# Optimization experiments

Hardware: AMD Instinct MI355X
Metric: run time of the kernel (lower is better)

The kernel has to match this reference:

```python
import jax, jax.numpy as jnp
import numpy as np
import math

N_HEADS = 32
N_KV_HEADS = 8
HEAD_DIM = 64
THETA = 10000.0
NEG_INF = -1e9


def _rope_cos_sin(seq_len, dim, dtype=jnp.float32):
    # freqs over even indices, matching torch.arange(0, dim, 2)/dim
    freqs = 1.0 / (THETA ** (jnp.arange(0, dim, 2, dtype=jnp.float32) / dim))  # [dim/2]
    angles = jnp.arange(seq_len, dtype=jnp.float32)[:, None] * freqs[None, :]  # [S, dim/2]
    return jnp.cos(angles).astype(dtype), jnp.sin(angles).astype(dtype)


def _apply_rope(x, cos, sin):
    # x: [B, S, H, D]; pairs (x[...,2i], x[...,2i+1]) rotated as complex numbers
    xr = x[..., 0::2]
    xi = x[..., 1::2]
    # broadcast cos/sin [S, D/2] -> [1, S, 1, D/2]
    c = cos[None, :, None, :]
    s = sin[None, :, None, :]
    or_ = xr * c - xi * s
    oi_ = xr * s + xi * c
    # interleave back: [..., D/2, 2] -> [..., D]
    return jnp.stack([or_, oi_], axis=-1).reshape(x.shape)


def setup_inputs() -> dict:
    key = jax.random.key(0)
    ks = jax.random.split(key, 5)
    B, S, D = 2, 2048, 2048
    KV_D = N_KV_HEADS * HEAD_DIM
    x = jax.random.normal(ks[0], (B, S, D), dtype=jnp.float32)
    sc = 1.0 / math.sqrt(D)
    wq = jax.random.normal(ks[1], (D, D), dtype=jnp.float32) * sc
    wk = jax.random.normal(ks[2], (D, KV_D), dtype=jnp.float32) * sc
    wv = jax.random.normal(ks[3], (D, KV_D), dtype=jnp.float32) * sc
    wo = jax.random.normal(ks[4], (D, D), dtype=jnp.float32) * sc
    # additive causal mask [1, 1, S, S]
    causal = jnp.tril(jnp.ones((S, S), dtype=bool))
    mask = jnp.where(causal, 0.0, NEG_INF).astype(jnp.float32)[None, None]
    return {"x": x, "mask": mask, "wq": wq, "wk": wk, "wv": wv, "wo": wo}


def reference(x, mask, wq, wk, wv, wo):
    B, S, D = x.shape
    n_rep = N_HEADS // N_KV_HEADS
    q = (x @ wq).reshape(B, S, N_HEADS, HEAD_DIM)
    k = (x @ wk).reshape(B, S, N_KV_HEADS, HEAD_DIM)
    v = (x @ wv).reshape(B, S, N_KV_HEADS, HEAD_DIM)
    cos, sin = _rope_cos_sin(S, HEAD_DIM)
    q = _apply_rope(q, cos, sin)
    k = _apply_rope(k, cos, sin)
    # GQA: repeat_interleave kv heads along head dim
    k = jnp.repeat(k, n_rep, axis=2)  # [B, S, H, D]
    v = jnp.repeat(v, n_rep, axis=2)
    scores = jnp.einsum("bqhd,bkhd->bhqk", q, k) / math.sqrt(HEAD_DIM)
    scores = scores + mask
    probs = jax.nn.softmax(scores.astype(jnp.float32), axis=-1).astype(q.dtype)
    out = jnp.einsum("bhqk,bkhd->bqhd", probs, v).reshape(B, S, N_HEADS * HEAD_DIM)
    return out @ wo
```

## Files before the change

kernel.cpp:

```cpp
#include <hip/hip_runtime.h>
#include <hip/hip_bf16.h>


#define S_LEN 2048
#define BATCH 2
#define D_MODEL 2048
#define NH 32
#define NKV 8
#define HD 64
#define KV_D (NKV * HD)
#define QKV_N (D_MODEL + 2 * KV_D)

typedef __attribute__((ext_vector_type(8))) short short8;
typedef __attribute__((ext_vector_type(4))) float float4v;
typedef __attribute__((ext_vector_type(16))) float f32x16;
typedef __attribute__((ext_vector_type(2))) unsigned uint2v;

typedef __attribute__((address_space(1))) const unsigned int gu32;
typedef __attribute__((address_space(3))) unsigned int lu32;

#if __has_builtin(__builtin_amdgcn_exp2f)
#define PEXP(x) __builtin_amdgcn_exp2f(x)
#else
#define PEXP(x) __expf((x) * 0.69314718f)
#endif
#define QSCALE 0.18033688f

__device__ __forceinline__ float bf2f(unsigned short u) {
    unsigned x = ((unsigned)u) << 16;
    return __builtin_bit_cast(float, x);
}
__device__ __forceinline__ unsigned short f2bf(float f) {
    unsigned u = __builtin_bit_cast(unsigned, f);
    unsigned r = (u + 0x7fffu + ((u >> 16) & 1u)) >> 16;
    return (unsigned short)r;
}

__device__ __forceinline__ unsigned cvt_pk_bf16(float a, float b) {
    unsigned r;
    asm("v_cvt_pk_bf16_f32 %0, %1, %2" : "=v"(r) : "v"(a), "v"(b));
    return r;
}

__device__ __forceinline__ void pl32swap(unsigned a, unsigned b,
                                         unsigned& x, unsigned& y) {
#if __has_builtin(__builtin_amdgcn_permlane32_swap)
    uint2v r = __builtin_amdgcn_permlane32_swap(a, b, false, false);
    x = r[0];
    y = r[1];
#else
    unsigned pa = (unsigned)__shfl_xor((int)a, 32);
    unsigned pb = (unsigned)__shfl_xor((int)b, 32);
    bool lo = (threadIdx.x & 63) < 32;
    x = lo ? a : pb;
    y = lo ? pa : b;
#endif
}

__global__ __launch_bounds__(256) void prep(const float* __restrict__ x,
                                            const float* __restrict__ wq,
                                            const float* __restrict__ wk,
                                            const float* __restrict__ wv,
                                            const float* __restrict__ wo,
                                            unsigned short* __restrict__ xb,
                                            unsigned short* __restrict__ wqkvT,
                                            unsigned short* __restrict__ woT) {
    __shared__ unsigned short t[32 * 33];
    const int bx = blockIdx.x;
    if (bx >= 10240) {
        long i = ((long)(bx - 10240) * 256 + threadIdx.x) * 4;
        const long n = (long)BATCH * S_LEN * D_MODEL;
        if (i + 3 >= n) return;
        const float4v v = *(const float4v*)&x[i];
        unsigned short o[4];
        o[0] = f2bf(v[0]); o[1] = f2bf(v[1]); o[2] = f2bf(v[2]); o[3] = f2bf(v[3]);
        *(__attribute__((ext_vector_type(4))) short*)&xb[i] =
            *(__attribute__((ext_vector_type(4))) short*)o;
        return;
    }
    const float* in;
    unsigned short* out;
    int N, nb, kb;
    if (bx < 4096) {
        in = wq; out = wqkvT; N = 2048;
        nb = (bx & 63) * 32; kb = (bx >> 6) * 32;
    } else if (bx < 5120) {
        const int i2 = bx - 4096;
        in = wk; out = wqkvT + (long)D_MODEL * D_MODEL; N = 512;
        nb = (i2 & 15) * 32; kb = (i2 >> 4) * 32;
    } else if (bx < 6144) {
        const int i2 = bx - 5120;
        in = wv; out = wqkvT + (long)(D_MODEL + KV_D) * D_MODEL; N = 512;
        nb = (i2 & 15) * 32; kb = (i2 >> 4) * 32;
    } else {
        const int i2 = bx - 6144;
        in = wo; out = woT; N = 2048;
        nb = (i2 & 63) * 32; kb = (i2 >> 6) * 32;
    }
    const int c = threadIdx.x & 31, rr = threadIdx.x >> 5;
#pragma unroll
    for (int it = 0; it < 4; ++it) {
        int r = it * 8 + rr;
        t[c * 33 + r] = f2bf(in[(long)(kb + r) * N + nb + c]);
    }
    __syncthreads();
#pragma unroll
    for (int it = 0; it < 4; ++it) {
        int r = it * 8 + rr;
        out[(long)(nb + r) * D_MODEL + kb + c] = t[r * 33 + c];
    }
}

template <int TM, bool F32OUT>
__global__ __launch_bounds__(256, TM == 64 ? 4 : 3)
void gemm_sw(const unsigned short* __restrict__ A,
             const unsigned short* __restrict__ BT,
             void* __restrict__ Cv, int M, int N, int K) {
    __shared__ unsigned short As[TM * 64];
    __shared__ unsigned short Bs[128 * 64];
    const int tid = threadIdx.x;
    const int wid = tid >> 6, lane = tid & 63;
    const int l15 = lane & 15, quad = lane >> 4;
    const int wm = (wid >> 1) * (TM / 2), wn = (wid & 1) * 64;
    const int row0 = blockIdx.x * TM, col0 = blockIdx.y * 128;
    constexpr int MI = TM / 32;

    float4v acc[MI][4];
    float4v z;
    z[0] = z[1] = z[2] = z[3] = 0.0f;
    for (int mi = 0; mi < MI; ++mi)
        for (int ni = 0; ni < 4; ++ni) acc[mi][ni] = z;

    const int r_ld = lane >> 3;
    const int swz_ld = ((lane & 7) ^ (lane >> 3)) * 8;
    const int sw = l15 & 7;

    for (int kb = 0; kb < K; kb += 64) {
        __syncthreads();
#pragma unroll
        for (int c = 0; c < 4; ++c) {
            int chunk = c * 4 + wid;
            int r = chunk * 8 + r_ld;
            __builtin_amdgcn_global_load_lds(
                (gu32*)&BT[(long)(col0 + r) * K + kb + swz_ld],
                (lu32*)&Bs[chunk * 512], 16, 0, 0);
            if (c < MI)
                __builtin_amdgcn_global_load_lds(
                    (gu32*)&A[(long)(row0 + r) * K + kb + swz_ld],
                    (lu32*)&As[chunk * 512], 16, 0, 0);
        }
        __syncthreads();
#pragma unroll
        for (int kk = 0; kk < 64; kk += 32) {
            short8 af[MI], bf[4];
#pragma unroll
            for (int i = 0; i < MI; ++i)
                af[i] = *(const short8*)
                    &As[(wm + i * 16 + l15) * 64 + ((((kk >> 3) + quad) ^ sw) << 3)];
#pragma unroll
            for (int i = 0; i < 4; ++i)
                bf[i] = *(const short8*)
                    &Bs[(wn + i * 16 + l15) * 64 + ((((kk >> 3) + quad) ^ sw) << 3)];
#pragma unroll
            for (int mi = 0; mi < MI; ++mi)
#pragma unroll
                for (int ni = 0; ni < 4; ++ni)
                    acc[mi][ni] = __builtin_amdgcn_mfma_f32_16x16x32_bf16(
                        af[mi], bf[ni], acc[mi][ni], 0, 0, 0);
        }
    }
#pragma unroll
    for (int mi = 0; mi < MI; ++mi)
#pragma unroll
        for (int ni = 0; ni < 4; ++ni)
#pragma unroll
            for (int r = 0; r < 4; ++r) {
                int m = row0 + wm + mi * 16 + quad * 4 + r;
                int n = col0 + wn + ni * 16 + l15;
                if (F32OUT)
                    ((float*)Cv)[(long)m * N + n] = acc[mi][ni][r];
                else
                    ((unsigned short*)Cv)[(long)m * N + n] = f2bf(acc[mi][ni][r]);
            }
}

__global__ __launch_bounds__(256) void rope_vtrans(unsigned short* __restrict__ qkv,
                                                   unsigned short* __restrict__ Vt) {
    __shared__ unsigned t[64 * 33];
    const int bx = blockIdx.x, tid = threadIdx.x;
    if (bx < 512) {
        const int i = tid & 31;
        const int row = bx * 8 + (tid >> 5);
        const int s = row & (S_LEN - 1);
        float freq = __expf(-0.28782313f * (float)i);
        float ang = (float)s * freq;
        float c = cosf(ang), sn = sinf(ang);
        unsigned* p = (unsigned*)qkv + ((long)row * QKV_N + 2 * i) / 2;
#pragma unroll
        for (int head = 0; head < 40; ++head) {
            const float qs = (head < 32) ? QSCALE : 1.0f;
            unsigned v = p[head * 32];
            float xr = bf2f((unsigned short)(v & 0xffff));
            float xi = bf2f((unsigned short)(v >> 16));
            unsigned short lo = f2bf((xr * c - xi * sn) * qs);
            unsigned short hi = f2bf((xr * sn + xi * c) * qs);
            p[head * 32] = (unsigned)lo | ((unsigned)hi << 16);
        }
        return;
    }
    const int idx = bx - 512;
    const int st = (idx & 31) * 64, kh = (idx >> 5) & 7, b = idx >> 8;
    {
        const int r2 = tid >> 3, dbase = (tid & 7) * 8;
        const unsigned short* src =
            qkv + ((long)(b * S_LEN + st + 2 * r2)) * QKV_N + D_MODEL + KV_D + kh * HD + dbase;
        short8 lo = *(const short8*)src;
        short8 hi = *(const short8*)(src + QKV_N);
#pragma unroll
        for (int j = 0; j < 8; ++j)
            t[(dbase + j) * 33 + r2] =
                (unsigned)(unsigned short)lo[j] | ((unsigned)(unsigned short)hi[j] << 16);
    }
    __syncthreads();
    {
        const int d = tid >> 2, sb = (tid & 3) * 8;
        unsigned short o[16];
#pragma unroll
        for (int jj = 0; jj < 8; ++jj) {
            unsigned v = t[d * 33 + sb + jj];
            o[2 * jj] = (unsigned short)(v & 0xffff);
            o[2 * jj + 1] = (unsigned short)(v >> 16);
        }
        unsigned short* dst =
            Vt + ((long)((b * 8 + kh) * 64 + d)) * S_LEN + st + sb * 2;
        *(short8*)dst = *(short8*)&o[0];
        *(short8*)(dst + 8) = *(short8*)&o[8];
    }
}

__global__ __launch_bounds__(512, 4) void flash8(const unsigned short* __restrict__ qkv,
                                                 const unsigned short* __restrict__ Vt,
                                                 unsigned short* __restrict__ O) {
    __shared__ unsigned short Ks[4][64 * 64];
    __shared__ unsigned short Vs[4][64 * 64];

    const int tid = threadIdx.x, w = tid >> 6, lane = tid & 63;
    const int g = w & 3, p = w >> 2;
    const int l31 = lane & 31, hi = lane >> 5;
    const int r7 = l31 & 7;
    const int h = blockIdx.y, b = blockIdx.z;
    const int kh = h >> 2, bkh = b * 8 + kh;
    const int qtA = blockIdx.x;

    const int sr = lane >> 3;
    const int sc = ((lane & 7) ^ sr) * 8;
    const unsigned short* Kg =
        qkv + (long)b * S_LEN * QKV_N + D_MODEL + kh * HD + sc;
    const unsigned short* Vg = Vt + ((long)bkh * 64) * S_LEN + sc;

#define STAGE8(pb)                                                                   \
    do {                                                                             \
        const int tt = (pb) + p;                                                     \
        const int bt = tt & 3;                                                       \
        const long kk0 = (long)tt * 64;                                              \
        __builtin_amdgcn_global_load_lds(                                            \
            (gu32*)&Kg[(kk0 + g * 16 + sr) * QKV_N],                                 \
            (lu32*)&Ks[bt][(g * 16) * 64], 16, 0, 0);                                \
        __builtin_amdgcn_global_load_lds(                                            \
            (gu32*)&Kg[(kk0 + g * 16 + 8 + sr) * QKV_N],                             \
            (lu32*)&Ks[bt][(g * 16 + 8) * 64], 16, 0, 0);                            \
        __builtin_amdgcn_global_load_lds(                                            \
            (gu32*)&Vg[(long)(g * 16 + sr) * S_LEN + kk0],                           \
            (lu32*)&Vs[bt][(g * 16) * 64], 16, 0, 0);                                \
        __builtin_amdgcn_global_load_lds(                                            \
            (gu32*)&Vg[(long)(g * 16 + 8 + sr) * S_LEN + kk0],                       \
            (lu32*)&Vs[bt][(g * 16 + 8) * 64], 16, 0, 0);                            \
    } while (0)

    for (int tsel = 0; tsel < 2; ++tsel) {
        const int qt = tsel ? (15 - qtA) : qtA;
        const int row_w = qt * 128 + g * 32;
        const int nkt = 2 * qt + 2;
        const int nss = nkt >> 1;

        short8 aq[4];
        {
            const long qbase = ((long)(b * S_LEN) + row_w + l31) * QKV_N + h * HD + hi * 8;
#pragma unroll
            for (int ks = 0; ks < 4; ++ks) aq[ks] = *(const short8*)&qkv[qbase + ks * 16];
        }

        f32x16 oacc[2] = {};
        float lp = 0.0f;

        STAGE8(0);
        __syncthreads();

        for (int ss = 0; ss < nss; ++ss) {
            const int t = 2 * ss + p;
            const int k0 = t * 64;
            const int bt = t & 3;
            if (2 * ss + 2 < nkt) STAGE8(2 * ss + 2);

            if (row_w + 31 >= k0) {
                const bool mb = (k0 + 63 > row_w);
#pragma unroll
                for (int kb2 = 0; kb2 < 2; ++kb2) {
                    short8 kf[4];
#pragma unroll
                    for (int ks = 0; ks < 4; ++ks)
                        kf[ks] = *(const short8*)
                            &Ks[bt][(kb2 * 32 + l31) * 64 + (((ks * 2 + hi) ^ r7) << 3)];
                    f32x16 s = {};
                    __builtin_amdgcn_s_setprio(1);
#pragma unroll
                    for (int ks = 0; ks < 4; ++ks)
                        s = __builtin_amdgcn_mfma_f32_32x32x16_bf16(kf[ks], aq[ks], s, 0, 0, 0);
                    __builtin_amdgcn_s_setprio(0);

                    const int qrel = row_w + l31 - k0 - kb2 * 32 - 4 * hi;
#pragma unroll
                    for (int r = 0; r < 16; ++r) {
                        float v = s[r];
                        if (mb && ((r & 3) + 8 * (r >> 2) > qrel)) v = -1e4f;
                        float pv = PEXP(v);
                        lp += pv;
                        s[r] = pv;
                    }

#pragma unroll
                    for (int ksl = 0; ksl < 2; ++ksl) {
                        const int gx = ksl * 8;
                        unsigned ca = cvt_pk_bf16(s[gx + 0], s[gx + 1]);
                        unsigned cb = cvt_pk_bf16(s[gx + 2], s[gx + 3]);
                        unsigned cc = cvt_pk_bf16(s[gx + 4], s[gx + 5]);
                        unsigned cd = cvt_pk_bf16(s[gx + 6], s[gx + 7]);
                        unsigned dw0, dw1, dw2, dw3;
                        pl32swap(ca, cc, dw0, dw2);
                        pl32swap(cb, cd, dw1, dw3);
                        union { unsigned u[4]; short8 v8; } pf;
                        pf.u[0] = dw0; pf.u[1] = dw1; pf.u[2] = dw2; pf.u[3] = dw3;
                        const int lc = kb2 * 4 + ksl * 2 + hi;
                        __builtin_amdgcn_s_setprio(1);
#pragma unroll
                        for (int dblk = 0; dblk < 2; ++dblk) {
                            short8 vf = *(const short8*)
                                &Vs[bt][(dblk * 32 + l31) * 64 + ((lc ^ r7) << 3)];
                            oacc[dblk] = __builtin_amdgcn_mfma_f32_32x32x16_bf16(
                                vf, pf.v8, oacc[dblk], 0, 0, 0);
                        }
                        __builtin_amdgcn_s_setprio(0);
                    }
                }
            }
            __syncthreads();
        }

        float* mV = (float*)&Vs[0][0];
        float* mL = (float*)&Ks[2][0];
        if (p == 1) {
#pragma unroll
            for (int dblk = 0; dblk < 2; ++dblk)
#pragma unroll
                for (int r = 0; r < 16; ++r)
                    mV[(g * 32 + dblk * 16 + r) * 64 + lane] = oacc[dblk][r];
            mL[g * 64 + lane] = lp;
        }
        __syncthreads();
        if (p == 0) {
#pragma unroll
            for (int dblk = 0; dblk < 2; ++dblk)
#pragma unroll
                for (int r = 0; r < 16; ++r)
                    oacc[dblk][r] += mV[(g * 32 + dblk * 16 + r) * 64 + lane];
            lp += mL[g * 64 + lane];

            float linv = 1.0f / (lp + __shfl_xor(lp, 32));
            unsigned short* Oe = &Ks[0][0] + g * 2048;
#pragma unroll
            for (int dblk = 0; dblk < 2; ++dblk)
#pragma unroll
                for (int rq = 0; rq < 4; ++rq) {
                    unsigned plo = cvt_pk_bf16(oacc[dblk][rq * 4 + 0] * linv,
                                               oacc[dblk][rq * 4 + 1] * linv);
                    unsigned phi = cvt_pk_bf16(oacc[dblk][rq * 4 + 2] * linv,
                                               oacc[dblk][rq * 4 + 3] * linv);
                    uint2v wv;
                    wv[0] = plo; wv[1] = phi;
                    int e = l31 * 64 + (((rq + 4 * dblk) ^ r7) << 3) + hi * 4;
                    *(uint2v*)&Oe[e] = wv;
                }
#pragma unroll
            for (int i = 0; i < 4; ++i) {
                int q2 = i * 8 + (lane >> 3);
                int e = q2 * 64 + (((lane & 7) ^ (lane >> 3)) << 3);
                short8 ov = *(const short8*)&Oe[e];
                long orow = ((long)(b * S_LEN) + row_w + q2) * D_MODEL + h * HD + (lane & 7) * 8;
                *(short8*)&O[orow] = ov;
            }
        }
        __syncthreads();
    }
#undef STAGE8
}

extern "C" void kernel_launch(void* const* d_in, const int* in_sizes, int n_in,
                              void* d_out, int out_size, void* d_ws, size_t ws_size,
                              hipStream_t stream) {
    const float* x  = (const float*)d_in[0];
    const float* wq = (const float*)d_in[n_in - 4];
    const float* wk = (const float*)d_in[n_in - 3];
    const float* wv = (const float*)d_in[n_in - 2];
    const float* wo = (const float*)d_in[n_in - 1];
    float* out = (float*)d_out;

    unsigned short* ws    = (unsigned short*)d_ws;
    unsigned short* xb    = ws;
    unsigned short* Obuf  = ws;
    unsigned short* qkv   = xb + (long)BATCH * S_LEN * D_MODEL;
    unsigned short* woT   = qkv + (long)BATCH * S_LEN * QKV_N;
    unsigned short* wqkvT = woT + (long)D_MODEL * D_MODEL;
    unsigned short* Vt    = wqkvT;

    const int M = BATCH * S_LEN;

    prep<<<18432, 256, 0, stream>>>(x, wq, wk, wv, wo, xb, wqkvT, woT);

    gemm_sw<128, false><<<dim3(M / 128, QKV_N / 128), 256, 0, stream>>>(
        xb, wqkvT, qkv, M, QKV_N, D_MODEL);

    rope_vtrans<<<1024, 256, 0, stream>>>(qkv, Vt);

    flash8<<<dim3(8, NH, BATCH), 512, 0, stream>>>(qkv, Vt, Obuf);

    gemm_sw<128, true><<<dim3(M / 128, D_MODEL / 128), 256, 0, stream>>>(
        Obuf, woT, out, M, D_MODEL, D_MODEL);
}
```

Baseline: 289.2 us.

## Split flash attention KV tiles across four wave groups with tree reduction

```diff
diff --git a/kernel.cpp b/kernel.cpp
--- a/kernel.cpp
+++ b/kernel.cpp
@@ -238,11 +238,11 @@
     }
 }
 
-__global__ __launch_bounds__(512, 4) void flash8(const unsigned short* __restrict__ qkv,
-                                                 const unsigned short* __restrict__ Vt,
-                                                 unsigned short* __restrict__ O) {
-    __shared__ unsigned short Ks[4][64 * 64];
-    __shared__ unsigned short Vs[4][64 * 64];
+__global__ __launch_bounds__(1024, 8) void flash10(const unsigned short* __restrict__ qkv,
+                                                   const unsigned short* __restrict__ Vt,
+                                                   unsigned short* __restrict__ O) {
+    __shared__ unsigned short SM[8 * 4096];
+    __shared__ float mLs[768];
 
     const int tid = threadIdx.x, w = tid >> 6, lane = tid & 63;
     const int g = w & 3, p = w >> 2;
@@ -257,31 +257,14 @@
     const unsigned short* Kg =
         qkv + (long)b * S_LEN * QKV_N + D_MODEL + kh * HD + sc;
     const unsigned short* Vg = Vt + ((long)bkh * 64) * S_LEN + sc;
-
-#define STAGE8(pb)                                                                   \
-    do {                                                                             \
-        const int tt = (pb) + p;                                                     \
-        const int bt = tt & 3;                                                       \
-        const long kk0 = (long)tt * 64;                                              \
-        __builtin_amdgcn_global_load_lds(                                            \
-            (gu32*)&Kg[(kk0 + g * 16 + sr) * QKV_N],                                 \
-            (lu32*)&Ks[bt][(g * 16) * 64], 16, 0, 0);                                \
-        __builtin_amdgcn_global_load_lds(                                            \
-            (gu32*)&Kg[(kk0 + g * 16 + 8 + sr) * QKV_N],                             \
-            (lu32*)&Ks[bt][(g * 16 + 8) * 64], 16, 0, 0);                            \
-        __builtin_amdgcn_global_load_lds(                                            \
-            (gu32*)&Vg[(long)(g * 16 + sr) * S_LEN + kk0],                           \
-            (lu32*)&Vs[bt][(g * 16) * 64], 16, 0, 0);                                \
-        __builtin_amdgcn_global_load_lds(                                            \
-            (gu32*)&Vg[(long)(g * 16 + 8 + sr) * S_LEN + kk0],                       \
-            (lu32*)&Vs[bt][(g * 16 + 8) * 64], 16, 0, 0);                            \
-    } while (0)
+    unsigned short* const KB = &SM[p * 4096];
+    unsigned short* const VB = &SM[16384 + p * 4096];
 
     for (int tsel = 0; tsel < 2; ++tsel) {
         const int qt = tsel ? (15 - qtA) : qtA;
         const int row_w = qt * 128 + g * 32;
         const int nkt = 2 * qt + 2;
-        const int nss = nkt >> 1;
+        const int nss = (nkt + 3) >> 2;
 
         short8 aq[4];
         {
@@ -293,16 +276,27 @@
         f32x16 oacc[2] = {};
         float lp = 0.0f;
 
-        STAGE8(0);
-        __syncthreads();
-
         for (int ss = 0; ss < nss; ++ss) {
-            const int t = 2 * ss + p;
+            const int t = 4 * ss + p;
             const int k0 = t * 64;
-            const int bt = t & 3;
-            if (2 * ss + 2 < nkt) STAGE8(2 * ss + 2);
-
-            if (row_w + 31 >= k0) {
+            if (t < nkt) {
+                const long kk0 = (long)t * 64;
+                __builtin_amdgcn_global_load_lds(
+                    (gu32*)&Kg[(kk0 + g * 16 + sr) * QKV_N],
+                    (lu32*)&KB[(g * 16) * 64], 16, 0, 0);
+                __builtin_amdgcn_global_load_lds(
+                    (gu32*)&Kg[(kk0 + g * 16 + 8 + sr) * QKV_N],
+                    (lu32*)&KB[(g * 16 + 8) * 64], 16, 0, 0);
+                __builtin_amdgcn_global_load_lds(
+                    (gu32*)&Vg[(long)(g * 16 + sr) * S_LEN + kk0],
+                    (lu32*)&VB[(g * 16) * 64], 16, 0, 0);
+                __builtin_amdgcn_global_load_lds(
+                    (gu32*)&Vg[(long)(g * 16 + 8 + sr) * S_LEN + kk0],
+                    (lu32*)&VB[(g * 16 + 8) * 64], 16, 0, 0);
+            }
+            __syncthreads();
+
+            if (t < nkt && row_w + 31 >= k0) {
                 const bool mb = (k0 + 63 > row_w);
 #pragma unroll
                 for (int kb2 = 0; kb2 < 2; ++kb2) {
@@ -310,7 +304,7 @@
 #pragma unroll
                     for (int ks = 0; ks < 4; ++ks)
                         kf[ks] = *(const short8*)
-                            &Ks[bt][(kb2 * 32 + l31) * 64 + (((ks * 2 + hi) ^ r7) << 3)];
+                            &KB[(kb2 * 32 + l31) * 64 + (((ks * 2 + hi) ^ r7) << 3)];
                     f32x16 s = {};
                     __builtin_amdgcn_s_setprio(1);
 #pragma unroll
@@ -345,7 +339,7 @@
 #pragma unroll
                         for (int dblk = 0; dblk < 2; ++dblk) {
                             short8 vf = *(const short8*)
-                                &Vs[bt][(dblk * 32 + l31) * 64 + ((lc ^ r7) << 3)];
+                                &VB[(dblk * 32 + l31) * 64 + ((lc ^ r7) << 3)];
                             oacc[dblk] = __builtin_amdgcn_mfma_f32_32x32x16_bf16(
                                 vf, pf.v8, oacc[dblk], 0, 0, 0);
                         }
@@ -356,15 +350,38 @@
             __syncthreads();
         }
 
-        float* mV = (float*)&Vs[0][0];
-        float* mL = (float*)&Ks[2][0];
+        float* mVbig = (float*)&SM[0];
+        if (p >= 1) mLs[(p - 1) * 256 + g * 64 + lane] = lp;
+        if (p >= 2) {
+            const int sl = (p - 2) * 8192;
+#pragma unroll
+            for (int dblk = 0; dblk < 2; ++dblk)
+#pragma unroll
+                for (int r = 0; r < 16; ++r)
+                    mVbig[sl + g * 2048 + (dblk * 16 + r) * 64 + lane] = oacc[dblk][r];
+        }
+        __syncthreads();
+        if (p == 0) {
+#pragma unroll
+            for (int dblk = 0; dblk < 2; ++dblk)
+#pragma unroll
+                for (int r = 0; r < 16; ++r)
+                    oacc[dblk][r] += mVbig[g * 2048 + (dblk * 16 + r) * 64 + lane];
+            lp += mLs[g * 64 + lane] + mLs[256 + g * 64 + lane] + mLs[512 + g * 64 + lane];
+        } else if (p == 1) {
+#pragma unroll
+            for (int dblk = 0; dblk < 2; ++dblk)
+#pragma unroll
+                for (int r = 0; r < 16; ++r)
+                    oacc[dblk][r] += mVbig[8192 + g * 2048 + (dblk * 16 + r) * 64 + lane];
+        }
+        __syncthreads();
         if (p == 1) {
 #pragma unroll
             for (int dblk = 0; dblk < 2; ++dblk)
 #pragma unroll
                 for (int r = 0; r < 16; ++r)
-                    mV[(g * 32 + dblk * 16 + r) * 64 + lane] = oacc[dblk][r];
-            mL[g * 64 + lane] = lp;
+                    mVbig[g * 2048 + (dblk * 16 + r) * 64 + lane] = oacc[dblk][r];
         }
         __syncthreads();
         if (p == 0) {
@@ -372,11 +389,10 @@
             for (int dblk = 0; dblk < 2; ++dblk)
 #pragma unroll
                 for (int r = 0; r < 16; ++r)
-                    oacc[dblk][r] += mV[(g * 32 + dblk * 16 + r) * 64 + lane];
-            lp += mL[g * 64 + lane];
+                    oacc[dblk][r] += mVbig[g * 2048 + (dblk * 16 + r) * 64 + lane];
 
             float linv = 1.0f / (lp + __shfl_xor(lp, 32));
-            unsigned short* Oe = &Ks[0][0] + g * 2048;
+            unsigned short* Oe = &SM[16384 + g * 2048];
 #pragma unroll
             for (int dblk = 0; dblk < 2; ++dblk)
 #pragma unroll
@@ -401,7 +417,6 @@
         }
         __syncthreads();
     }
-#undef STAGE8
 }
 
 extern "C" void kernel_launch(void* const* d_in, const int* in_sizes, int n_in,
@@ -431,7 +446,7 @@
 
     rope_vtrans<<<1024, 256, 0, stream>>>(qkv, Vt);
 
-    flash8<<<dim3(8, NH, BATCH), 512, 0, stream>>>(qkv, Vt, Obuf);
+    flash10<<<dim3(8, NH, BATCH), 1024, 0, stream>>>(qkv, Vt, Obuf);
 
     gemm_sw<128, true><<<dim3(M / 128, D_MODEL / 128), 256, 0, stream>>>(
         Obuf, woT, out, M, D_MODEL, D_MODEL);
```

Result: slower. 747.6 us (+158.5%).
